# Performance work log

Measured on AMD Instinct MI355X. Metric: run time of the kernel, lower is better.

The kernel has to match this reference:

```python
import jax, jax.numpy as jnp
import numpy as np

D_IN = 1024
D_OUT = 1024
NUM_HEADS = 16
D_HEAD = D_OUT // NUM_HEADS


def setup_inputs() -> dict:
    key = jax.random.key(0)
    ks = jax.random.split(key, 6)
    s = 0.02
    return {
        "x": jax.random.normal(ks[0], (2, 2048, D_IN), dtype=jnp.float32),
        "W_q": jax.random.normal(ks[1], (D_IN, D_OUT), dtype=jnp.float32) * s,
        "W_k": jax.random.normal(ks[2], (D_IN, D_OUT), dtype=jnp.float32) * s,
        "W_v": jax.random.normal(ks[3], (D_IN, D_OUT), dtype=jnp.float32) * s,
        "W_o": jax.random.normal(ks[4], (D_OUT, D_OUT), dtype=jnp.float32) * s,
        "b_o": jax.random.normal(ks[5], (D_OUT,), dtype=jnp.float32) * s,
    }


def reference(x, W_q, W_k, W_v, W_o, b_o):
    B, T, _ = x.shape
    # qkv projections (no bias), split heads -> [B, H, T, d_head]
    def split_heads(t):
        return t.reshape(B, T, NUM_HEADS, D_HEAD).transpose(0, 2, 1, 3)
    q = split_heads(x @ W_q)
    k = split_heads(x @ W_k)
    v = split_heads(x @ W_v)
    # full causal scores [B, H, T, T]
    scores = jnp.einsum("bhqd,bhkd->bhqk", q, k)
    causal = jnp.triu(jnp.ones((T, T), dtype=bool), k=1)
    scores = jnp.where(causal, -jnp.inf, scores)
    attn = jax.nn.softmax(scores / np.sqrt(D_HEAD).astype(np.float32), axis=-1)
    # dropout rate is 0.0 -> identity
    ctx = jnp.einsum("bhqk,bhkd->bhqd", attn, v)
    ctx = ctx.transpose(0, 2, 1, 3).reshape(B, T, D_OUT)
    return ctx @ W_o + b_o
```

## Files before the change

kernel.cpp:

```cpp
#include <hip/hip_runtime.h>
#include <hip/hip_bf16.h>
#include <cstdint>

#define SEQ_T 2048
#define DMODEL 1024
#define NHEAD 16
#define DHEAD 64

typedef __attribute__((ext_vector_type(8))) __bf16 bf16x8;
typedef __attribute__((ext_vector_type(4))) float floatx4;
typedef __attribute__((ext_vector_type(16))) float floatx16;
typedef __attribute__((ext_vector_type(2))) unsigned uint32x2;

static __device__ __forceinline__ uint16_t f2bf(float f) {
    union { float f; uint32_t u; } v; v.f = f;
    uint32_t r = v.u + 0x7FFFu + ((v.u >> 16) & 1u);
    return (uint16_t)(r >> 16);
}

static __device__ __forceinline__ uint32_t pack2bf(float a, float b) {
    union { __bf16 h[2]; uint32_t u; } p;
    p.h[0] = (__bf16)a; p.h[1] = (__bf16)b;
    return p.u;
}

__global__ void mha_cvt(const float* __restrict__ x, uint16_t* __restrict__ xb,
                        const float* __restrict__ W0, const float* __restrict__ W1,
                        const float* __restrict__ W2, const float* __restrict__ W3,
                        uint16_t* __restrict__ T0, uint16_t* __restrict__ T1,
                        uint16_t* __restrict__ T2, uint16_t* __restrict__ T3) {
    if (blockIdx.z == 4) {
        int base = (blockIdx.y * 16 + blockIdx.x) * 256 + threadIdx.x;
#pragma unroll
        for (int i = 0; i < 16; ++i) {
            int idx = base + i * 65536;
            float4 f = ((const float4*)x)[idx];
            union { uint16_t u[4]; uint64_t v; } o;
            o.u[0] = f2bf(f.x); o.u[1] = f2bf(f.y); o.u[2] = f2bf(f.z); o.u[3] = f2bf(f.w);
            ((uint64_t*)xb)[idx] = o.v;
        }
        return;
    }
    const float* W; uint16_t* Tt; float sc;
    switch (blockIdx.z) {
        case 0: W = W0; Tt = T0; sc = 0.125f * 1.44269504089f; break;
        case 1: W = W1; Tt = T1; sc = 1.f; break;
        case 2: W = W2; Tt = T2; sc = 1.f; break;
        default: W = W3; Tt = T3; sc = 1.f; break;
    }
    __shared__ float tile[64][65];
    const int c  = threadIdx.x & 63;
    const int r0 = threadIdx.x >> 6;
    const int R0 = blockIdx.y * 64, C0 = blockIdx.x * 64;
#pragma unroll
    for (int rr = 0; rr < 16; ++rr) {
        int r = r0 + rr * 4;
        tile[r][c] = W[(size_t)(R0 + r) * DMODEL + C0 + c];
    }
    __syncthreads();
#pragma unroll
    for (int rr = 0; rr < 16; ++rr) {
        int r = r0 + rr * 4;
        Tt[(size_t)(C0 + r) * DMODEL + R0 + c] = f2bf(tile[c][r] * sc);
    }
}

template<int MODE>
__device__ __forceinline__ void gemm_bk64_body(
    const uint16_t* __restrict__ A, const uint16_t* __restrict__ Bt,
    uint16_t* __restrict__ outB) {
    const int K = DMODEL, N = DMODEL;
    extern __shared__ char smem[];
    uint16_t* As = (uint16_t*)smem;
    uint16_t* Bs = (uint16_t*)(smem + 8192);
    const int tid  = threadIdx.x;
    const int wave = tid >> 6;
    const int lane = tid & 63;
    const int m0 = blockIdx.y * 64;
    const int n0 = blockIdx.x * 128;
    const int lr   = lane & 15;
    const int quad = lane >> 4;

    floatx4 acc[4][2];
#pragma unroll
    for (int i = 0; i < 4; ++i)
#pragma unroll
        for (int j = 0; j < 2; ++j) acc[i][j] = (floatx4)0.0f;

    for (int k0 = 0; k0 < K; k0 += 64) {
#pragma unroll
        for (int i = 0; i < 2; ++i) {
            int c = i * 256 + tid;
            int r = c >> 3, s = (c & 7) ^ (r & 7);
            const uint16_t* g = A + (size_t)(m0 + r) * K + k0 + s * 8;
            __builtin_amdgcn_global_load_lds((const __attribute__((address_space(1))) void*)g,
                                             (__attribute__((address_space(3))) void*)(As + (size_t)c * 8), 16, 0, 0);
        }
#pragma unroll
        for (int i = 0; i < 4; ++i) {
            int c = i * 256 + tid;
            int r = c >> 3, s = (c & 7) ^ (r & 7);
            const uint16_t* g = Bt + (size_t)(n0 + r) * K + k0 + s * 8;
            __builtin_amdgcn_global_load_lds((const __attribute__((address_space(1))) void*)g,
                                             (__attribute__((address_space(3))) void*)(Bs + (size_t)c * 8), 16, 0, 0);
        }
        __syncthreads();
#pragma unroll
        for (int ks = 0; ks < 2; ++ks) {
            bf16x8 af[4], bfr[2];
#pragma unroll
            for (int mi = 0; mi < 4; ++mi) {
                int row = mi * 16 + lr;
                af[mi] = *(const bf16x8*)&As[row * 64 + (((ks * 4 + quad) ^ (row & 7)) << 3)];
            }
#pragma unroll
            for (int ni = 0; ni < 2; ++ni) {
                int row = wave * 32 + ni * 16 + lr;
                bfr[ni] = *(const bf16x8*)&Bs[row * 64 + (((ks * 4 + quad) ^ (row & 7)) << 3)];
            }
#pragma unroll
            for (int mi = 0; mi < 4; ++mi)
#pragma unroll
                for (int ni = 0; ni < 2; ++ni)
                    acc[mi][ni] = __builtin_amdgcn_mfma_f32_16x16x32_bf16(af[mi], bfr[ni], acc[mi][ni], 0, 0, 0);
        }
        __syncthreads();
    }
    if constexpr (MODE == 1) {
        uint16_t* Ct = (uint16_t*)smem;
        const int bb = m0 >> 11, t0 = m0 & 2047;
#pragma unroll
        for (int mi = 0; mi < 4; ++mi)
#pragma unroll
            for (int ni = 0; ni < 2; ++ni) {
                int cl = wave * 32 + ni * 16 + lr;
                int tl = mi * 16 + quad * 4;
                int tls = tl ^ ((cl & 3) << 4);
                union { uint16_t u[4]; uint64_t v8; } pk;
#pragma unroll
                for (int r = 0; r < 4; ++r) pk.u[r] = f2bf(acc[mi][ni][r]);
                *(uint64_t*)&Ct[cl * 72 + tls] = pk.v8;
            }
        __syncthreads();
#pragma unroll
        for (int k = 0; k < 4; ++k) {
            int c = k * 256 + tid;
            int cl = c >> 3, off = (c & 7) * 8;
            int offs = off ^ ((cl & 3) << 4);
            uint4 v = *(const uint4*)&Ct[cl * 72 + offs];
            *(uint4*)&outB[((size_t)(bb * 1024 + n0 + cl)) * 2048 + t0 + off] = v;
        }
    } else {
#pragma unroll
        for (int mi = 0; mi < 4; ++mi)
#pragma unroll
            for (int ni = 0; ni < 2; ++ni) {
                int col = n0 + wave * 32 + ni * 16 + lr;
#pragma unroll
                for (int r = 0; r < 4; ++r) {
                    int row = m0 + mi * 16 + quad * 4 + r;
                    outB[(size_t)row * N + col] = f2bf(acc[mi][ni][r]);
                }
            }
    }
}

__global__ __launch_bounds__(256) void mha_gemm_qkv(
    const uint16_t* __restrict__ A,
    const uint16_t* __restrict__ Wq, const uint16_t* __restrict__ Wk, const uint16_t* __restrict__ Wv,
    uint16_t* __restrict__ Q, uint16_t* __restrict__ K, uint16_t* __restrict__ Vt) {
    switch (blockIdx.z) {
        case 0:  gemm_bk64_body<0>(A, Wq, Q);  break;
        case 1:  gemm_bk64_body<0>(A, Wk, K);  break;
        default: gemm_bk64_body<1>(A, Wv, Vt); break;
    }
}

__global__ __launch_bounds__(512) void mha_gemm_out(
    const uint16_t* __restrict__ A, const uint16_t* __restrict__ Wot,
    float* __restrict__ out, const float* __restrict__ bias) {
    const int K = DMODEL, N = DMODEL;
    extern __shared__ char smem[];
    uint16_t* As = (uint16_t*)smem;
    uint16_t* Bs = (uint16_t*)(smem + 8192);
    const int tid  = threadIdx.x;
    const int wave = tid >> 6;
    const int lane = tid & 63;
    const int m0 = blockIdx.y * 64;
    const int n0 = blockIdx.x * 128;
    const int lr   = lane & 15;
    const int quad = lane >> 4;
    const int wm = wave >> 2, wn = wave & 3;

    floatx4 acc[2][2];
#pragma unroll
    for (int i = 0; i < 2; ++i)
#pragma unroll
        for (int j = 0; j < 2; ++j) acc[i][j] = (floatx4)0.0f;

    for (int k0 = 0; k0 < K; k0 += 64) {
        {
            int c = tid;
            int r = c >> 3, s = (c & 7) ^ (r & 7);
            const uint16_t* g = A + (size_t)(m0 + r) * K + k0 + s * 8;
            __builtin_amdgcn_global_load_lds((const __attribute__((address_space(1))) void*)g,
                                             (__attribute__((address_space(3))) void*)(As + (size_t)c * 8), 16, 0, 0);
        }
#pragma unroll
        for (int i = 0; i < 2; ++i) {
            int c = i * 512 + tid;
            int r = c >> 3, s = (c & 7) ^ (r & 7);
            const uint16_t* g = Wot + (size_t)(n0 + r) * K + k0 + s * 8;
            __builtin_amdgcn_global_load_lds((const __attribute__((address_space(1))) void*)g,
                                             (__attribute__((address_space(3))) void*)(Bs + (size_t)c * 8), 16, 0, 0);
        }
        __syncthreads();
#pragma unroll
        for (int ks = 0; ks < 2; ++ks) {
            bf16x8 af[2], bfr[2];
#pragma unroll
            for (int mi = 0; mi < 2; ++mi) {
                int row = wm * 32 + mi * 16 + lr;
                af[mi] = *(const bf16x8*)&As[row * 64 + (((ks * 4 + quad) ^ (row & 7)) << 3)];
            }
#pragma unroll
            for (int ni = 0; ni < 2; ++ni) {
                int row = wn * 32 + ni * 16 + lr;
                bfr[ni] = *(const bf16x8*)&Bs[row * 64 + (((ks * 4 + quad) ^ (row & 7)) << 3)];
            }
#pragma unroll
            for (int mi = 0; mi < 2; ++mi)
#pragma unroll
                for (int ni = 0; ni < 2; ++ni)
                    acc[mi][ni] = __builtin_amdgcn_mfma_f32_16x16x32_bf16(af[mi], bfr[ni], acc[mi][ni], 0, 0, 0);
        }
        __syncthreads();
    }
#pragma unroll
    for (int mi = 0; mi < 2; ++mi)
#pragma unroll
        for (int ni = 0; ni < 2; ++ni) {
            int col = n0 + wn * 32 + ni * 16 + lr;
            float bv = bias[col];
#pragma unroll
            for (int r = 0; r < 4; ++r) {
                int row = m0 + wm * 32 + mi * 16 + quad * 4 + r;
                out[(size_t)row * N + col] = acc[mi][ni][r] + bv;
            }
        }
}

__global__ __launch_bounds__(1024, 1) void mha_attn_mfma(
    const uint16_t* __restrict__ Q, const uint16_t* __restrict__ K,
    const uint16_t* __restrict__ Vt, uint16_t* __restrict__ ctx) {
    extern __shared__ char asmem[];
    uint16_t* Ks0 = (uint16_t*)asmem;
    uint16_t* Vs0 = (uint16_t*)(asmem + 32768);
    float*    lbuf = (float*)(asmem + 65536);

    const int tid  = threadIdx.x;
    const int wave = tid >> 6;
    const int lane = tid & 63;
    const int l31  = lane & 31;
    const int hi   = lane >> 5;
    const int l7   = lane & 7;
    const int qg   = wave & 3;
    const int kvq  = wave >> 2;
    const int h = blockIdx.x;
    const int p = blockIdx.y;
    const int b = blockIdx.z;
    const int jH = 15 - p, jL = p;
    const int TH = jH + 1;

    const uint16_t* kg;
    const uint16_t* vg;
    {
        int c = tid;
        int rk = c >> 3, ck = c & 7;
        kg = K + ((size_t)(b * SEQ_T) + rk) * DMODEL + h * DHEAD + ((ck ^ (rk & 7)) * 8);
        int rv = c >> 4, cv = c & 15;
        int sv = (cv & 8) | ((cv & 7) ^ (rv & 7));
        vg = Vt + ((size_t)(b * 1024 + h * DHEAD + rv)) * 2048 + sv * 8;
    }

    int q0w = jH * 128 + qg * 32;
    bf16x8 qf[4];
    auto load_q = [&]() {
        const uint16_t* qb = Q + ((size_t)(b * SEQ_T) + q0w + l31) * DMODEL + h * DHEAD;
#pragma unroll
        for (int f = 0; f < 4; ++f)
            qf[f] = *(const bf16x8*)(qb + f * 16 + hi * 8);
    };
    load_q();

    floatx16 o[2];
#pragma unroll
    for (int dt = 0; dt < 2; ++dt) o[dt] = (floatx16)0.0f;
    float lac = 0.f;

    auto stage = [&](int kv0, int buf) {
        __builtin_amdgcn_global_load_lds(
            (const __attribute__((address_space(1))) void*)(kg + (size_t)kv0 * DMODEL),
            (__attribute__((address_space(3))) void*)(Ks0 + buf * 8192 + tid * 8), 16, 0, 0);
        __builtin_amdgcn_global_load_lds(
            (const __attribute__((address_space(1))) void*)(vg + kv0),
            (__attribute__((address_space(3))) void*)(Vs0 + buf * 8192 + tid * 8), 16, 0, 0);
    };

    auto halfsum = [&](float x) -> float {
#if __has_builtin(__builtin_amdgcn_permlane32_swap)
        uint32x2 r = __builtin_amdgcn_permlane32_swap(__float_as_uint(x), __float_as_uint(x), false, false);
        return __uint_as_float(r.x) + __uint_as_float(r.y);
#else
        return x + __shfl_xor(x, 32, 64);
#endif
    };

    auto combine_store = [&](int cur) {
        __syncthreads();
        float* osc = (qg < 2) ? (float*)(Ks0 + cur * 8192)
                              : (float*)(Vs0 + cur * 8192);
        const int qoff = (qg & 1) * 32;
        float lt = halfsum(lac);
#pragma unroll
        for (int pass = 3; pass >= 1; --pass) {
            if (kvq == pass) {
                if (pass == 3) {
#pragma unroll
                    for (int dt = 0; dt < 2; ++dt)
#pragma unroll
                        for (int r = 0; r < 16; ++r) {
                            int row = (r & 3) + 8 * (r >> 2) + 4 * hi;
                            osc[(qoff + row) * 64 + dt * 32 + l31] = o[dt][r];
                        }
                    if (lane < 32) lbuf[qg * 32 + lane] = lt;
                } else {
#pragma unroll
                    for (int dt = 0; dt < 2; ++dt)
#pragma unroll
                        for (int r = 0; r < 16; ++r) {
                            int row = (r & 3) + 8 * (r >> 2) + 4 * hi;
                            osc[(qoff + row) * 64 + dt * 32 + l31] += o[dt][r];
                        }
                    if (lane < 32) lbuf[qg * 32 + lane] += lt;
                }
            }
            __syncthreads();
        }
        if (kvq == 0) {
            float ltot = lt + lbuf[qg * 32 + l31];
            if (lane < 32) lbuf[128 + qg * 32 + lane] = 1.f / ltot;
#pragma unroll
            for (int dt = 0; dt < 2; ++dt)
#pragma unroll
                for (int r = 0; r < 16; ++r) {
                    int row = (r & 3) + 8 * (r >> 2) + 4 * hi;
                    float ov = o[dt][r] + osc[(qoff + row) * 64 + dt * 32 + l31];
                    float li = lbuf[128 + qg * 32 + row];
                    size_t addr = ((size_t)(b * SEQ_T) + q0w + row) * DMODEL + h * DHEAD + dt * 32 + l31;
                    ctx[addr] = f2bf(ov * li);
                }
        }
    };

    stage(0, 0);
    __syncthreads();

    for (int t = 0; t < 17; ++t) {
        const int cur = t & 1;
        const int kv0 = (t < TH ? t : t - TH) * 128;
        if (t + 1 < 17) {
            int tn = t + 1;
            stage((tn < TH ? tn : tn - TH) * 128, tn & 1);
        }
        const uint16_t* Kc = Ks0 + cur * 8192;
        const uint16_t* Vc = Vs0 + cur * 8192;
        const int kb = kv0 + kvq * 32;
        floatx16 s = (floatx16)0.0f;
        __builtin_amdgcn_s_setprio(1);
#pragma unroll
        for (int f = 0; f < 4; ++f) {
            bf16x8 kf = *(const bf16x8*)&Kc[(kvq * 32 + l31) * 64 + (((2 * f + hi) ^ l7) << 3)];
            s = __builtin_amdgcn_mfma_f32_32x32x16_bf16(kf, qf[f], s, 0, 0, 0);
        }
        __builtin_amdgcn_s_setprio(0);
        if (kb + 31 > q0w) {
            int qr = q0w + l31;
#pragma unroll
            for (int r = 0; r < 16; ++r) {
                int k = kb + (r & 3) + 8 * (r >> 2) + 4 * hi;
                if (k > qr) s[r] = -3e38f;
            }
        }
        uint32_t d0[2], d1[2], d2[2], d3[2];
#pragma unroll
        for (int i = 0; i < 2; ++i) {
            float a, c2;
            a = __builtin_amdgcn_exp2f(s[2 * i]);      c2 = __builtin_amdgcn_exp2f(s[2 * i + 1]);
            lac += a + c2; d0[i] = pack2bf(a, c2);
            a = __builtin_amdgcn_exp2f(s[4 + 2 * i]);  c2 = __builtin_amdgcn_exp2f(s[4 + 2 * i + 1]);
            lac += a + c2; d1[i] = pack2bf(a, c2);
            a = __builtin_amdgcn_exp2f(s[8 + 2 * i]);  c2 = __builtin_amdgcn_exp2f(s[8 + 2 * i + 1]);
            lac += a + c2; d2[i] = pack2bf(a, c2);
            a = __builtin_amdgcn_exp2f(s[12 + 2 * i]); c2 = __builtin_amdgcn_exp2f(s[12 + 2 * i + 1]);
            lac += a + c2; d3[i] = pack2bf(a, c2);
        }
        bf16x8 paf[2];
#if __has_builtin(__builtin_amdgcn_permlane32_swap)
        {
            uint32x2 r0 = __builtin_amdgcn_permlane32_swap(d0[0], d1[0], false, false);
            uint32x2 r1 = __builtin_amdgcn_permlane32_swap(d0[1], d1[1], false, false);
            union { uint32_t u[4]; bf16x8 v; } f0;
            f0.u[0] = r0.x; f0.u[1] = r1.x; f0.u[2] = r0.y; f0.u[3] = r1.y;
            paf[0] = f0.v;
            uint32x2 r2 = __builtin_amdgcn_permlane32_swap(d2[0], d3[0], false, false);
            uint32x2 r3 = __builtin_amdgcn_permlane32_swap(d2[1], d3[1], false, false);
            union { uint32_t u[4]; bf16x8 v; } f1;
            f1.u[0] = r2.x; f1.u[1] = r3.x; f1.u[2] = r2.y; f1.u[3] = r3.y;
            paf[1] = f1.v;
        }
#else
        {
            uint32_t s00 = __shfl_xor((int)d0[0], 32, 64), s01 = __shfl_xor((int)d0[1], 32, 64);
            uint32_t s10 = __shfl_xor((int)d1[0], 32, 64), s11 = __shfl_xor((int)d1[1], 32, 64);
            union { uint32_t u[4]; bf16x8 v; } f0;
            f0.u[0] = hi ? s10 : d0[0]; f0.u[1] = hi ? s11 : d0[1];
            f0.u[2] = hi ? d1[0] : s00; f0.u[3] = hi ? d1[1] : s01;
            paf[0] = f0.v;
            uint32_t s20 = __shfl_xor((int)d2[0], 32, 64), s21 = __shfl_xor((int)d2[1], 32, 64);
            uint32_t s30 = __shfl_xor((int)d3[0], 32, 64), s31 = __shfl_xor((int)d3[1], 32, 64);
            union { uint32_t u[4]; bf16x8 v; } f1;
            f1.u[0] = hi ? s30 : d2[0]; f1.u[1] = hi ? s31 : d2[1];
            f1.u[2] = hi ? d3[0] : s20; f1.u[3] = hi ? d3[1] : s21;
            paf[1] = f1.v;
        }
#endif
        __builtin_amdgcn_s_setprio(1);
#pragma unroll
        for (int f = 0; f < 2; ++f)
#pragma unroll
            for (int dt = 0; dt < 2; ++dt) {
                bf16x8 vf = *(const bf16x8*)&Vc[(dt * 32 + l31) * 128 + (((kvq * 4 + 2 * f + hi) ^ l7) << 3)];
                o[dt] = __builtin_amdgcn_mfma_f32_32x32x16_bf16(paf[f], vf, o[dt], 0, 0, 0);
            }
        __builtin_amdgcn_s_setprio(0);
        if (t == TH - 1) {
            combine_store(cur);
            q0w = jL * 128 + qg * 32;
            load_q();
#pragma unroll
            for (int dt = 0; dt < 2; ++dt) o[dt] = (floatx16)0.0f;
            lac = 0.f;
        }
        if (t + 1 < 17) __syncthreads();
    }
    combine_store(0);
}

extern "C" void kernel_launch(void* const* d_in, const int* in_sizes, int n_in,
                              void* d_out, int out_size, void* d_ws, size_t ws_size,
                              hipStream_t stream) {
    const float* x  = (const float*)d_in[0];
    const float* Wq = (const float*)d_in[1];
    const float* Wk = (const float*)d_in[2];
    const float* Wv = (const float*)d_in[3];
    const float* Wo = (const float*)d_in[4];
    const float* bo = (const float*)d_in[5];
    float* out = (float*)d_out;

    char* ws = (char*)d_ws;
    const size_t SZ_X = (size_t)4096 * DMODEL * 2;
    const size_t SZ_W = (size_t)DMODEL * DMODEL * 2;
    size_t off = 0;
    uint16_t* xb  = (uint16_t*)(ws + off); off += SZ_X;
    uint16_t* wqt = (uint16_t*)(ws + off); off += SZ_W;
    uint16_t* wkt = (uint16_t*)(ws + off); off += SZ_W;
    uint16_t* wvt = (uint16_t*)(ws + off); off += SZ_W;
    uint16_t* wot = (uint16_t*)(ws + off); off += SZ_W;
    uint16_t* Qb  = (uint16_t*)(ws + off); off += SZ_X;
    uint16_t* Kb  = (uint16_t*)(ws + off); off += SZ_X;
    uint16_t* Vtb = (uint16_t*)(ws + off); off += SZ_X;
    uint16_t* Cb  = (uint16_t*)(ws + off); off += SZ_X;
    (void)ws_size; (void)in_sizes; (void)n_in; (void)out_size;

    mha_cvt<<<dim3(16, 16, 5), 256, 0, stream>>>(x, xb, Wq, Wk, Wv, Wo, wqt, wkt, wvt, wot);
    mha_gemm_qkv<<<dim3(8, 64, 3), 256, 24576, stream>>>(xb, wqt, wkt, wvt, Qb, Kb, Vtb);
    mha_attn_mfma<<<dim3(NHEAD, 8, 2), 1024, 66560, stream>>>(Qb, Kb, Vtb, Cb);
    mha_gemm_out<<<dim3(8, 64), 512, 24576, stream>>>(Cb, wot, out, bo);
}
```

Baseline: 176.8 us.

## Halve attention block to 512 threads and triple-buffer K/V with vmcnt waits

The attention kernel now runs 8 waves per block instead of 16. Each wave processes two 32-key sub-tiles per 128-key step, so the cross-wave combine shrinks from three serialized passes to one. K/V staging moves from double to triple buffering with a prefetch distance of two, using explicit vmcnt waits plus s_barrier in place of __syncthreads. This aims to cut combine synchronization and hide load latency better. The cost is more LDS per block (about 97KB, which may cap occupancy at one block per CU despite the launch bounds) and fewer waves to hide latency.

```diff
diff --git a/kernel.cpp b/kernel.cpp
--- a/kernel.cpp
+++ b/kernel.cpp
@@ -250,13 +250,13 @@
         }
 }
 
-__global__ __launch_bounds__(1024, 1) void mha_attn_mfma(
+__global__ __launch_bounds__(512, 2) void mha_attn_mfma(
     const uint16_t* __restrict__ Q, const uint16_t* __restrict__ K,
     const uint16_t* __restrict__ Vt, uint16_t* __restrict__ ctx) {
     extern __shared__ char asmem[];
     uint16_t* Ks0 = (uint16_t*)asmem;
-    uint16_t* Vs0 = (uint16_t*)(asmem + 32768);
-    float*    lbuf = (float*)(asmem + 65536);
+    uint16_t* Vs0 = (uint16_t*)(asmem + 49152);
+    float*    lbuf = (float*)(asmem + 98304);
 
     const int tid  = threadIdx.x;
     const int wave = tid >> 6;
@@ -265,22 +265,24 @@
     const int hi   = lane >> 5;
     const int l7   = lane & 7;
     const int qg   = wave & 3;
-    const int kvq  = wave >> 2;
+    const int kvh  = wave >> 2;
     const int h = blockIdx.x;
     const int p = blockIdx.y;
     const int b = blockIdx.z;
     const int jH = 15 - p, jL = p;
     const int TH = jH + 1;
 
-    const uint16_t* kg;
-    const uint16_t* vg;
-    {
-        int c = tid;
+    const uint16_t* kg[2];
+    const uint16_t* vg[2];
+    int cch[2];
+#pragma unroll
+    for (int i = 0; i < 2; ++i) {
+        int c = i * 512 + tid; cch[i] = c;
         int rk = c >> 3, ck = c & 7;
-        kg = K + ((size_t)(b * SEQ_T) + rk) * DMODEL + h * DHEAD + ((ck ^ (rk & 7)) * 8);
+        kg[i] = K + ((size_t)(b * SEQ_T) + rk) * DMODEL + h * DHEAD + ((ck ^ (rk & 7)) * 8);
         int rv = c >> 4, cv = c & 15;
         int sv = (cv & 8) | ((cv & 7) ^ (rv & 7));
-        vg = Vt + ((size_t)(b * 1024 + h * DHEAD + rv)) * 2048 + sv * 8;
+        vg[i] = Vt + ((size_t)(b * 1024 + h * DHEAD + rv)) * 2048 + sv * 8;
     }
 
     int q0w = jH * 128 + qg * 32;
@@ -299,13 +301,19 @@
     float lac = 0.f;
 
     auto stage = [&](int kv0, int buf) {
-        __builtin_amdgcn_global_load_lds(
-            (const __attribute__((address_space(1))) void*)(kg + (size_t)kv0 * DMODEL),
-            (__attribute__((address_space(3))) void*)(Ks0 + buf * 8192 + tid * 8), 16, 0, 0);
-        __builtin_amdgcn_global_load_lds(
-            (const __attribute__((address_space(1))) void*)(vg + kv0),
-            (__attribute__((address_space(3))) void*)(Vs0 + buf * 8192 + tid * 8), 16, 0, 0);
+        uint16_t* kd = Ks0 + buf * 8192;
+        uint16_t* vd = Vs0 + buf * 8192;
+#pragma unroll
+        for (int i = 0; i < 2; ++i) {
+            __builtin_amdgcn_global_load_lds(
+                (const __attribute__((address_space(1))) void*)(kg[i] + (size_t)kv0 * DMODEL),
+                (__attribute__((address_space(3))) void*)(kd + cch[i] * 8), 16, 0, 0);
+            __builtin_amdgcn_global_load_lds(
+                (const __attribute__((address_space(1))) void*)(vg[i] + kv0),
+                (__attribute__((address_space(3))) void*)(vd + cch[i] * 8), 16, 0, 0);
+        }
     };
+    auto kvof = [&](int t) { return (t < TH ? t : t - TH) * 128; };
 
     auto halfsum = [&](float x) -> float {
 #if __has_builtin(__builtin_amdgcn_permlane32_swap)
@@ -322,32 +330,18 @@
                               : (float*)(Vs0 + cur * 8192);
         const int qoff = (qg & 1) * 32;
         float lt = halfsum(lac);
-#pragma unroll
-        for (int pass = 3; pass >= 1; --pass) {
-            if (kvq == pass) {
-                if (pass == 3) {
-#pragma unroll
-                    for (int dt = 0; dt < 2; ++dt)
-#pragma unroll
-                        for (int r = 0; r < 16; ++r) {
-                            int row = (r & 3) + 8 * (r >> 2) + 4 * hi;
-                            osc[(qoff + row) * 64 + dt * 32 + l31] = o[dt][r];
-                        }
-                    if (lane < 32) lbuf[qg * 32 + lane] = lt;
-                } else {
-#pragma unroll
-                    for (int dt = 0; dt < 2; ++dt)
-#pragma unroll
-                        for (int r = 0; r < 16; ++r) {
-                            int row = (r & 3) + 8 * (r >> 2) + 4 * hi;
-                            osc[(qoff + row) * 64 + dt * 32 + l31] += o[dt][r];
-                        }
-                    if (lane < 32) lbuf[qg * 32 + lane] += lt;
+        if (kvh == 1) {
+#pragma unroll
+            for (int dt = 0; dt < 2; ++dt)
+#pragma unroll
+                for (int r = 0; r < 16; ++r) {
+                    int row = (r & 3) + 8 * (r >> 2) + 4 * hi;
+                    osc[(qoff + row) * 64 + dt * 32 + l31] = o[dt][r];
                 }
-            }
-            __syncthreads();
-        }
-        if (kvq == 0) {
+            if (lane < 32) lbuf[qg * 32 + lane] = lt;
+        }
+        __syncthreads();
+        if (kvh == 0) {
             float ltot = lt + lbuf[qg * 32 + l31];
             if (lane < 32) lbuf[128 + qg * 32 + lane] = 1.f / ltot;
 #pragma unroll
@@ -363,87 +357,89 @@
         }
     };
 
-    stage(0, 0);
-    __syncthreads();
+    stage(kvof(0), 0);
+    stage(kvof(1), 1);
+    __builtin_amdgcn_s_waitcnt(0x0F74);
+    __builtin_amdgcn_s_barrier();
 
     for (int t = 0; t < 17; ++t) {
-        const int cur = t & 1;
-        const int kv0 = (t < TH ? t : t - TH) * 128;
-        if (t + 1 < 17) {
-            int tn = t + 1;
-            stage((tn < TH ? tn : tn - TH) * 128, tn & 1);
-        }
+        const int cur = t % 3;
+        const int kv0 = kvof(t);
+        if (t + 2 < 17) stage(kvof(t + 2), (t + 2) % 3);
         const uint16_t* Kc = Ks0 + cur * 8192;
         const uint16_t* Vc = Vs0 + cur * 8192;
-        const int kb = kv0 + kvq * 32;
-        floatx16 s = (floatx16)0.0f;
-        __builtin_amdgcn_s_setprio(1);
-#pragma unroll
-        for (int f = 0; f < 4; ++f) {
-            bf16x8 kf = *(const bf16x8*)&Kc[(kvq * 32 + l31) * 64 + (((2 * f + hi) ^ l7) << 3)];
-            s = __builtin_amdgcn_mfma_f32_32x32x16_bf16(kf, qf[f], s, 0, 0, 0);
-        }
-        __builtin_amdgcn_s_setprio(0);
-        if (kb + 31 > q0w) {
-            int qr = q0w + l31;
-#pragma unroll
-            for (int r = 0; r < 16; ++r) {
-                int k = kb + (r & 3) + 8 * (r >> 2) + 4 * hi;
-                if (k > qr) s[r] = -3e38f;
-            }
-        }
-        uint32_t d0[2], d1[2], d2[2], d3[2];
-#pragma unroll
-        for (int i = 0; i < 2; ++i) {
-            float a, c2;
-            a = __builtin_amdgcn_exp2f(s[2 * i]);      c2 = __builtin_amdgcn_exp2f(s[2 * i + 1]);
-            lac += a + c2; d0[i] = pack2bf(a, c2);
-            a = __builtin_amdgcn_exp2f(s[4 + 2 * i]);  c2 = __builtin_amdgcn_exp2f(s[4 + 2 * i + 1]);
-            lac += a + c2; d1[i] = pack2bf(a, c2);
-            a = __builtin_amdgcn_exp2f(s[8 + 2 * i]);  c2 = __builtin_amdgcn_exp2f(s[8 + 2 * i + 1]);
-            lac += a + c2; d2[i] = pack2bf(a, c2);
-            a = __builtin_amdgcn_exp2f(s[12 + 2 * i]); c2 = __builtin_amdgcn_exp2f(s[12 + 2 * i + 1]);
-            lac += a + c2; d3[i] = pack2bf(a, c2);
-        }
-        bf16x8 paf[2];
+#pragma unroll
+        for (int kt = 0; kt < 2; ++kt) {
+            const int kb = kv0 + kvh * 64 + kt * 32;
+            floatx16 s = (floatx16)0.0f;
+            __builtin_amdgcn_s_setprio(1);
+#pragma unroll
+            for (int f = 0; f < 4; ++f) {
+                bf16x8 kf = *(const bf16x8*)&Kc[(kvh * 64 + kt * 32 + l31) * 64 + (((2 * f + hi) ^ l7) << 3)];
+                s = __builtin_amdgcn_mfma_f32_32x32x16_bf16(kf, qf[f], s, 0, 0, 0);
+            }
+            __builtin_amdgcn_s_setprio(0);
+            if (kb + 31 > q0w) {
+                int qr = q0w + l31;
+#pragma unroll
+                for (int r = 0; r < 16; ++r) {
+                    int k = kb + (r & 3) + 8 * (r >> 2) + 4 * hi;
+                    if (k > qr) s[r] = -3e38f;
+                }
+            }
+            uint32_t d0[2], d1[2], d2[2], d3[2];
+#pragma unroll
+            for (int i = 0; i < 2; ++i) {
+                float a, c2;
+                a = __builtin_amdgcn_exp2f(s[2 * i]);      c2 = __builtin_amdgcn_exp2f(s[2 * i + 1]);
+                lac += a + c2; d0[i] = pack2bf(a, c2);
+                a = __builtin_amdgcn_exp2f(s[4 + 2 * i]);  c2 = __builtin_amdgcn_exp2f(s[4 + 2 * i + 1]);
+                lac += a + c2; d1[i] = pack2bf(a, c2);
+                a = __builtin_amdgcn_exp2f(s[8 + 2 * i]);  c2 = __builtin_amdgcn_exp2f(s[8 + 2 * i + 1]);
+                lac += a + c2; d2[i] = pack2bf(a, c2);
+                a = __builtin_amdgcn_exp2f(s[12 + 2 * i]); c2 = __builtin_amdgcn_exp2f(s[12 + 2 * i + 1]);
+                lac += a + c2; d3[i] = pack2bf(a, c2);
+            }
+            bf16x8 paf[2];
 #if __has_builtin(__builtin_amdgcn_permlane32_swap)
-        {
-            uint32x2 r0 = __builtin_amdgcn_permlane32_swap(d0[0], d1[0], false, false);
-            uint32x2 r1 = __builtin_amdgcn_permlane32_swap(d0[1], d1[1], false, false);
-            union { uint32_t u[4]; bf16x8 v; } f0;
-            f0.u[0] = r0.x; f0.u[1] = r1.x; f0.u[2] = r0.y; f0.u[3] = r1.y;
-            paf[0] = f0.v;
-            uint32x2 r2 = __builtin_amdgcn_permlane32_swap(d2[0], d3[0], false, false);
-            uint32x2 r3 = __builtin_amdgcn_permlane32_swap(d2[1], d3[1], false, false);
-            union { uint32_t u[4]; bf16x8 v; } f1;
-            f1.u[0] = r2.x; f1.u[1] = r3.x; f1.u[2] = r2.y; f1.u[3] = r3.y;
-            paf[1] = f1.v;
-        }
+            {
+                uint32x2 r0 = __builtin_amdgcn_permlane32_swap(d0[0], d1[0], false, false);
+                uint32x2 r1 = __builtin_amdgcn_permlane32_swap(d0[1], d1[1], false, false);
+                union { uint32_t u[4]; bf16x8 v; } f0;
+                f0.u[0] = r0.x; f0.u[1] = r1.x; f0.u[2] = r0.y; f0.u[3] = r1.y;
+                paf[0] = f0.v;
+                uint32x2 r2 = __builtin_amdgcn_permlane32_swap(d2[0], d3[0], false, false);
+                uint32x2 r3 = __builtin_amdgcn_permlane32_swap(d2[1], d3[1], false, false);
+                union { uint32_t u[4]; bf16x8 v; } f1;
+                f1.u[0] = r2.x; f1.u[1] = r3.x; f1.u[2] = r2.y; f1.u[3] = r3.y;
+                paf[1] = f1.v;
+            }
 #else
-        {
-            uint32_t s00 = __shfl_xor((int)d0[0], 32, 64), s01 = __shfl_xor((int)d0[1], 32, 64);
-            uint32_t s10 = __shfl_xor((int)d1[0], 32, 64), s11 = __shfl_xor((int)d1[1], 32, 64);
-            union { uint32_t u[4]; bf16x8 v; } f0;
-            f0.u[0] = hi ? s10 : d0[0]; f0.u[1] = hi ? s11 : d0[1];
-            f0.u[2] = hi ? d1[0] : s00; f0.u[3] = hi ? d1[1] : s01;
-            paf[0] = f0.v;
-            uint32_t s20 = __shfl_xor((int)d2[0], 32, 64), s21 = __shfl_xor((int)d2[1], 32, 64);
-            uint32_t s30 = __shfl_xor((int)d3[0], 32, 64), s31 = __shfl_xor((int)d3[1], 32, 64);
-            union { uint32_t u[4]; bf16x8 v; } f1;
-            f1.u[0] = hi ? s30 : d2[0]; f1.u[1] = hi ? s31 : d2[1];
-            f1.u[2] = hi ? d3[0] : s20; f1.u[3] = hi ? d3[1] : s21;
-            paf[1] = f1.v;
-        }
+            {
+                uint32_t s00 = __shfl_xor((int)d0[0], 32, 64), s01 = __shfl_xor((int)d0[1], 32, 64);
+                uint32_t s10 = __shfl_xor((int)d1[0], 32, 64), s11 = __shfl_xor((int)d1[1], 32, 64);
+                union { uint32_t u[4]; bf16x8 v; } f0;
+                f0.u[0] = hi ? s10 : d0[0]; f0.u[1] = hi ? s11 : d0[1];
+                f0.u[2] = hi ? d1[0] : s00; f0.u[3] = hi ? d1[1] : s01;
+                paf[0] = f0.v;
+                uint32_t s20 = __shfl_xor((int)d2[0], 32, 64), s21 = __shfl_xor((int)d2[1], 32, 64);
+                uint32_t s30 = __shfl_xor((int)d3[0], 32, 64), s31 = __shfl_xor((int)d3[1], 32, 64);
+                union { uint32_t u[4]; bf16x8 v; } f1;
+                f1.u[0] = hi ? s30 : d2[0]; f1.u[1] = hi ? s31 : d2[1];
+                f1.u[2] = hi ? d3[0] : s20; f1.u[3] = hi ? d3[1] : s21;
+                paf[1] = f1.v;
+            }
 #endif
-        __builtin_amdgcn_s_setprio(1);
-#pragma unroll
-        for (int f = 0; f < 2; ++f)
-#pragma unroll
-            for (int dt = 0; dt < 2; ++dt) {
-                bf16x8 vf = *(const bf16x8*)&Vc[(dt * 32 + l31) * 128 + (((kvq * 4 + 2 * f + hi) ^ l7) << 3)];
-                o[dt] = __builtin_amdgcn_mfma_f32_32x32x16_bf16(paf[f], vf, o[dt], 0, 0, 0);
-            }
-        __builtin_amdgcn_s_setprio(0);
+            __builtin_amdgcn_s_setprio(1);
+#pragma unroll
+            for (int f = 0; f < 2; ++f)
+#pragma unroll
+                for (int dt = 0; dt < 2; ++dt) {
+                    bf16x8 vf = *(const bf16x8*)&Vc[(dt * 32 + l31) * 128 + ((kvh * 8 + ((kt * 4 + 2 * f + hi) ^ l7)) << 3)];
+                    o[dt] = __builtin_amdgcn_mfma_f32_32x32x16_bf16(paf[f], vf, o[dt], 0, 0, 0);
+                }
+            __builtin_amdgcn_s_setprio(0);
+        }
         if (t == TH - 1) {
             combine_store(cur);
             q0w = jL * 128 + qg * 32;
@@ -452,9 +448,15 @@
             for (int dt = 0; dt < 2; ++dt) o[dt] = (floatx16)0.0f;
             lac = 0.f;
         }
-        if (t + 1 < 17) __syncthreads();
-    }
-    combine_store(0);
+        if (t + 2 < 17) {
+            __builtin_amdgcn_s_waitcnt(0x0F74);
+            __builtin_amdgcn_s_barrier();
+        } else if (t + 1 < 17) {
+            __builtin_amdgcn_s_waitcnt(0x0F70);
+            __builtin_amdgcn_s_barrier();
+        }
+    }
+    combine_store(16 % 3);
 }
 
 extern "C" void kernel_launch(void* const* d_in, const int* in_sizes, int n_in,
@@ -485,6 +487,6 @@
 
     mha_cvt<<<dim3(16, 16, 5), 256, 0, stream>>>(x, xb, Wq, Wk, Wv, Wo, wqt, wkt, wvt, wot);
     mha_gemm_qkv<<<dim3(8, 64, 3), 256, 24576, stream>>>(xb, wqt, wkt, wvt, Qb, Kb, Vtb);
-    mha_attn_mfma<<<dim3(NHEAD, 8, 2), 1024, 66560, stream>>>(Qb, Kb, Vtb, Cb);
+    mha_attn_mfma<<<dim3(NHEAD, 8, 2), 512, 99328, stream>>>(Qb, Kb, Vtb, Cb);
     mha_gemm_out<<<dim3(8, 64), 512, 24576, stream>>>(Cb, wot, out, bo);
 }
```

Result: faster. 168.9 us (-4.4%).

## Split attention KV tiles across two blocks and merge partials in separate kernel

Applied to the files above, without the earlier changes.

The attention kernel changes from 1024-thread blocks, where four waves split each 128-key tile, to 512-thread blocks with launch bounds allowing two blocks per CU. Each of the two blocks covers one 64-key half of every tile. The z grid dimension doubles so the two key halves run as separate blocks. Each writes unnormalized fp32 partial outputs and row sums to workspace, and a new merge kernel adds them, normalizes and converts to bf16. This shortens the in-block reduction and raises occupancy, at the cost of an extra kernel launch and a large fp32 round trip through global memory.

```diff
diff --git a/kernel.cpp b/kernel.cpp
--- a/kernel.cpp
+++ b/kernel.cpp
@@ -250,12 +250,14 @@
         }
 }
 
-__global__ __launch_bounds__(1024, 1) void mha_attn_mfma(
+__global__ __launch_bounds__(512, 2) void mha_attn_mfma(
     const uint16_t* __restrict__ Q, const uint16_t* __restrict__ K,
-    const uint16_t* __restrict__ Vt, uint16_t* __restrict__ ctx) {
+    const uint16_t* __restrict__ Vt, float* __restrict__ opart,
+    float* __restrict__ lpart) {
     extern __shared__ char asmem[];
     uint16_t* Ks0 = (uint16_t*)asmem;
-    uint16_t* Vs0 = (uint16_t*)(asmem + 32768);
+    uint16_t* Vs0 = (uint16_t*)(asmem + 16384);
+    float*    osc = (float*)(asmem + 32768);
     float*    lbuf = (float*)(asmem + 65536);
 
     const int tid  = threadIdx.x;
@@ -266,9 +268,10 @@
     const int l7   = lane & 7;
     const int qg   = wave & 3;
     const int kvq  = wave >> 2;
-    const int h = blockIdx.x;
-    const int p = blockIdx.y;
-    const int b = blockIdx.z;
+    const int h    = blockIdx.x;
+    const int p    = blockIdx.y;
+    const int kvhB = blockIdx.z >> 1;
+    const int b    = blockIdx.z & 1;
     const int jH = 15 - p, jL = p;
     const int TH = jH + 1;
 
@@ -277,10 +280,9 @@
     {
         int c = tid;
         int rk = c >> 3, ck = c & 7;
-        kg = K + ((size_t)(b * SEQ_T) + rk) * DMODEL + h * DHEAD + ((ck ^ (rk & 7)) * 8);
-        int rv = c >> 4, cv = c & 15;
-        int sv = (cv & 8) | ((cv & 7) ^ (rv & 7));
-        vg = Vt + ((size_t)(b * 1024 + h * DHEAD + rv)) * 2048 + sv * 8;
+        kg = K + ((size_t)(b * SEQ_T) + kvhB * 64 + rk) * DMODEL + h * DHEAD + ((ck ^ (rk & 7)) * 8);
+        int rv = c >> 3, cv = c & 7;
+        vg = Vt + ((size_t)(b * 1024 + h * DHEAD + rv)) * 2048 + kvhB * 64 + ((cv ^ (rv & 7)) * 8);
     }
 
     int q0w = jH * 128 + qg * 32;
@@ -301,11 +303,12 @@
     auto stage = [&](int kv0, int buf) {
         __builtin_amdgcn_global_load_lds(
             (const __attribute__((address_space(1))) void*)(kg + (size_t)kv0 * DMODEL),
-            (__attribute__((address_space(3))) void*)(Ks0 + buf * 8192 + tid * 8), 16, 0, 0);
+            (__attribute__((address_space(3))) void*)(Ks0 + buf * 4096 + tid * 8), 16, 0, 0);
         __builtin_amdgcn_global_load_lds(
             (const __attribute__((address_space(1))) void*)(vg + kv0),
-            (__attribute__((address_space(3))) void*)(Vs0 + buf * 8192 + tid * 8), 16, 0, 0);
+            (__attribute__((address_space(3))) void*)(Vs0 + buf * 4096 + tid * 8), 16, 0, 0);
     };
+    auto kvof = [&](int t) { return (t < TH ? t : t - TH) * 128; };
 
     auto halfsum = [&](float x) -> float {
 #if __has_builtin(__builtin_amdgcn_permlane32_swap)
@@ -316,66 +319,47 @@
 #endif
     };
 
-    auto combine_store = [&](int cur) {
-        __syncthreads();
-        float* osc = (qg < 2) ? (float*)(Ks0 + cur * 8192)
-                              : (float*)(Vs0 + cur * 8192);
-        const int qoff = (qg & 1) * 32;
+    auto combine_store = [&]() {
+        __syncthreads();
         float lt = halfsum(lac);
-#pragma unroll
-        for (int pass = 3; pass >= 1; --pass) {
-            if (kvq == pass) {
-                if (pass == 3) {
-#pragma unroll
-                    for (int dt = 0; dt < 2; ++dt)
-#pragma unroll
-                        for (int r = 0; r < 16; ++r) {
-                            int row = (r & 3) + 8 * (r >> 2) + 4 * hi;
-                            osc[(qoff + row) * 64 + dt * 32 + l31] = o[dt][r];
-                        }
-                    if (lane < 32) lbuf[qg * 32 + lane] = lt;
-                } else {
-#pragma unroll
-                    for (int dt = 0; dt < 2; ++dt)
-#pragma unroll
-                        for (int r = 0; r < 16; ++r) {
-                            int row = (r & 3) + 8 * (r >> 2) + 4 * hi;
-                            osc[(qoff + row) * 64 + dt * 32 + l31] += o[dt][r];
-                        }
-                    if (lane < 32) lbuf[qg * 32 + lane] += lt;
-                }
-            }
-            __syncthreads();
-        }
-        if (kvq == 0) {
-            float ltot = lt + lbuf[qg * 32 + l31];
-            if (lane < 32) lbuf[128 + qg * 32 + lane] = 1.f / ltot;
+        if (kvq == 1) {
 #pragma unroll
             for (int dt = 0; dt < 2; ++dt)
 #pragma unroll
                 for (int r = 0; r < 16; ++r) {
                     int row = (r & 3) + 8 * (r >> 2) + 4 * hi;
-                    float ov = o[dt][r] + osc[(qoff + row) * 64 + dt * 32 + l31];
-                    float li = lbuf[128 + qg * 32 + row];
-                    size_t addr = ((size_t)(b * SEQ_T) + q0w + row) * DMODEL + h * DHEAD + dt * 32 + l31;
-                    ctx[addr] = f2bf(ov * li);
+                    osc[(qg * 32 + row) * 64 + dt * 32 + l31] = o[dt][r];
                 }
+            if (lane < 32) lbuf[qg * 32 + lane] = lt;
+        }
+        __syncthreads();
+        if (kvq == 0) {
+            float* op = opart + (size_t)kvhB * (4096u * 1024u);
+            if (lane < 32) {
+                float ltot = lt + lbuf[qg * 32 + lane];
+                lpart[((size_t)(kvhB * 2 + b) * SEQ_T + q0w + lane) * NHEAD + h] = ltot;
+            }
+#pragma unroll
+            for (int dt = 0; dt < 2; ++dt)
+#pragma unroll
+                for (int r = 0; r < 16; ++r) {
+                    int row = (r & 3) + 8 * (r >> 2) + 4 * hi;
+                    float ov = o[dt][r] + osc[(qg * 32 + row) * 64 + dt * 32 + l31];
+                    op[((size_t)(b * SEQ_T) + q0w + row) * DMODEL + h * DHEAD + dt * 32 + l31] = ov;
+                }
         }
     };
 
-    stage(0, 0);
+    stage(kvof(0), 0);
     __syncthreads();
 
     for (int t = 0; t < 17; ++t) {
         const int cur = t & 1;
-        const int kv0 = (t < TH ? t : t - TH) * 128;
-        if (t + 1 < 17) {
-            int tn = t + 1;
-            stage((tn < TH ? tn : tn - TH) * 128, tn & 1);
-        }
-        const uint16_t* Kc = Ks0 + cur * 8192;
-        const uint16_t* Vc = Vs0 + cur * 8192;
-        const int kb = kv0 + kvq * 32;
+        const int kv0 = kvof(t);
+        if (t + 1 < 17) stage(kvof(t + 1), (t + 1) & 1);
+        const uint16_t* Kc = Ks0 + cur * 4096;
+        const uint16_t* Vc = Vs0 + cur * 4096;
+        const int kb = kv0 + kvhB * 64 + kvq * 32;
         floatx16 s = (floatx16)0.0f;
         __builtin_amdgcn_s_setprio(1);
 #pragma unroll
@@ -440,12 +424,12 @@
         for (int f = 0; f < 2; ++f)
 #pragma unroll
             for (int dt = 0; dt < 2; ++dt) {
-                bf16x8 vf = *(const bf16x8*)&Vc[(dt * 32 + l31) * 128 + (((kvq * 4 + 2 * f + hi) ^ l7) << 3)];
+                bf16x8 vf = *(const bf16x8*)&Vc[(dt * 32 + l31) * 64 + (((kvq * 4 + 2 * f + hi) ^ l7) << 3)];
                 o[dt] = __builtin_amdgcn_mfma_f32_32x32x16_bf16(paf[f], vf, o[dt], 0, 0, 0);
             }
         __builtin_amdgcn_s_setprio(0);
         if (t == TH - 1) {
-            combine_store(cur);
+            combine_store();
             q0w = jL * 128 + qg * 32;
             load_q();
 #pragma unroll
@@ -454,7 +438,32 @@
         }
         if (t + 1 < 17) __syncthreads();
     }
-    combine_store(0);
+    combine_store();
+}
+
+__global__ __launch_bounds__(256) void mha_merge(
+    const float* __restrict__ opart, const float* __restrict__ lpart,
+    uint16_t* __restrict__ ctx) {
+    const float* o0 = opart;
+    const float* o1 = opart + (size_t)4096 * 1024;
+    int base = blockIdx.x * 256 + threadIdx.x;
+#pragma unroll
+    for (int i = 0; i < 2; ++i) {
+        int cidx = base + i * 524288;
+        int row = cidx >> 8;
+        int hh  = (cidx & 255) >> 4;
+        float l0 = lpart[(size_t)row * NHEAD + hh];
+        float l1 = lpart[((size_t)4096 + row) * NHEAD + hh];
+        float linv = 1.f / (l0 + l1);
+        float4 a = ((const float4*)o0)[cidx];
+        float4 c = ((const float4*)o1)[cidx];
+        union { uint16_t u[4]; uint64_t v; } pk;
+        pk.u[0] = f2bf((a.x + c.x) * linv);
+        pk.u[1] = f2bf((a.y + c.y) * linv);
+        pk.u[2] = f2bf((a.z + c.z) * linv);
+        pk.u[3] = f2bf((a.w + c.w) * linv);
+        ((uint64_t*)ctx)[cidx] = pk.v;
+    }
 }
 
 extern "C" void kernel_launch(void* const* d_in, const int* in_sizes, int n_in,
@@ -481,10 +490,13 @@
     uint16_t* Kb  = (uint16_t*)(ws + off); off += SZ_X;
     uint16_t* Vtb = (uint16_t*)(ws + off); off += SZ_X;
     uint16_t* Cb  = (uint16_t*)(ws + off); off += SZ_X;
+    float* opart  = (float*)(ws + off);    off += (size_t)2 * 4096 * 1024 * 4;
+    float* lpart  = (float*)(ws + off);    off += (size_t)2 * 4096 * NHEAD * 4;
     (void)ws_size; (void)in_sizes; (void)n_in; (void)out_size;
 
     mha_cvt<<<dim3(16, 16, 5), 256, 0, stream>>>(x, xb, Wq, Wk, Wv, Wo, wqt, wkt, wvt, wot);
     mha_gemm_qkv<<<dim3(8, 64, 3), 256, 24576, stream>>>(xb, wqt, wkt, wvt, Qb, Kb, Vtb);
-    mha_attn_mfma<<<dim3(NHEAD, 8, 2), 1024, 66560, stream>>>(Qb, Kb, Vtb, Cb);
+    mha_attn_mfma<<<dim3(NHEAD, 8, 4), 512, 66560, stream>>>(Qb, Kb, Vtb, opart, lpart);
+    mha_merge<<<dim3(2048), 256, 0, stream>>>(opart, lpart, Cb);
     mha_gemm_out<<<dim3(8, 64), 512, 24576, stream>>>(Cb, wot, out, bo);
 }
```

Result: no change. 179.0 us (+1.3%).
